# Kernel optimization log

Hardware: AMD Instinct MI355X
Metric: run time of the kernel (lower is better)

Reference implementation:

```python
import jax, jax.numpy as jnp
import numpy as np

B, L, C = 2, 2048, 1024
H = 16
D = C // H  # 64
MAX_SCALE_MUL = float(np.log(100.0))
EPS = 1e-12


def setup_inputs() -> dict:
    key = jax.random.key(0)
    ks = jax.random.split(key, 6)
    x = jax.random.normal(ks[0], (B, L, C), dtype=jnp.float32)
    attn_bias = jax.random.normal(ks[1], (1, 1, L, L), dtype=jnp.float32) * 0.02
    W_qkv = jax.random.normal(ks[2], (3 * C, C), dtype=jnp.float32) * (1.0 / np.sqrt(C))
    q_bias = jnp.zeros((C,), dtype=jnp.float32)
    v_bias = jnp.zeros((C,), dtype=jnp.float32)
    scale_mul = jnp.full((1, H, 1, 1), np.log(4.0), dtype=jnp.float32)
    W_proj = jax.random.normal(ks[3], (C, C), dtype=jnp.float32) * (1.0 / np.sqrt(C))
    b_proj = jnp.zeros((C,), dtype=jnp.float32)
    return {"x": x, "attn_bias": attn_bias, "W_qkv": W_qkv, "q_bias": q_bias,
            "v_bias": v_bias, "scale_mul": scale_mul, "W_proj": W_proj, "b_proj": b_proj}


def _l2norm(t):
    # F.normalize(dim=-1): x / max(||x||_2, eps)
    n = jnp.sqrt(jnp.sum(t * t, axis=-1, keepdims=True))
    return t / jnp.maximum(n, EPS)


def reference(x, attn_bias, W_qkv, q_bias, v_bias, scale_mul, W_proj, b_proj):
    bias = jnp.concatenate([q_bias, jnp.zeros_like(q_bias), v_bias])  # (3C,)
    qkv = x @ W_qkv.T + bias                     # (B, L, 3C)
    qkv = qkv.reshape(B, L, 3, H, D)
    q, k, v = jnp.moveaxis(qkv, 2, 0)            # each (B, L, H, D)
    q = jnp.transpose(q, (0, 2, 1, 3))           # (B, H, L, D)
    k = jnp.transpose(k, (0, 2, 1, 3))
    v = jnp.transpose(v, (0, 2, 1, 3))
    # attn_l2_norm path: scale = 1, learned per-head scale clamped at log(100)
    sm = jnp.exp(jnp.minimum(scale_mul, MAX_SCALE_MUL))  # (1, H, 1, 1)
    q = _l2norm(q) * sm
    k = _l2norm(k)
    scores = jnp.einsum('bhqd,bhkd->bhqk', q, k) + attn_bias  # scale=1
    attn = jax.nn.softmax(scores, axis=-1)
    out = jnp.einsum('bhqk,bhkd->bhqd', attn, v)  # (B, H, L, D)
    out = jnp.transpose(out, (0, 2, 1, 3)).reshape(B, L, C)
    return out @ W_proj.T + b_proj
```

## Files before the change

### kernel.cpp

```cpp
#include <hip/hip_runtime.h>


typedef __bf16 bf16x8 __attribute__((ext_vector_type(8)));
typedef __bf16 bf16x4 __attribute__((ext_vector_type(4)));
typedef float  f32x4  __attribute__((ext_vector_type(4)));

#define BB 2
#define LL 2048
#define CC 1024
#define HH 16
#define DD 64
#define LOG2E 1.44269504088896f

__device__ __forceinline__ f32x4 mfma_16x16x32(bf16x8 a, bf16x8 b, f32x4 c) {
    return __builtin_amdgcn_mfma_f32_16x16x32_bf16(a, b, c, 0, 0, 0);
}

__device__ __forceinline__ void gload_lds16(const __bf16* g, __bf16* lds) {
    __builtin_amdgcn_global_load_lds(
        (const __attribute__((address_space(1))) unsigned int*)g,
        (__attribute__((address_space(3))) unsigned int*)lds,
        16, 0, 0);
}

__device__ __forceinline__ unsigned pk_bf16(float a, float b) {
    unsigned short ua = __builtin_bit_cast(unsigned short, (__bf16)a);
    unsigned short ub = __builtin_bit_cast(unsigned short, (__bf16)b);
    return (unsigned)ua | ((unsigned)ub << 16);
}

__global__ __launch_bounds__(256) void cvt3_kernel(
    const float* __restrict__ x, const float* __restrict__ wq, const float* __restrict__ wp,
    __bf16* __restrict__ xb, __bf16* __restrict__ wqb, __bf16* __restrict__ wpb) {
    const int i = blockIdx.x * 256 + threadIdx.x;
    const float* src; __bf16* dst; int off;
    if (i < 1048576)      { src = x;  dst = xb;  off = i; }
    else if (i < 1835008) { src = wq; dst = wqb; off = i - 1048576; }
    else                  { src = wp; dst = wpb; off = i - 1835008; }
    float4 v = reinterpret_cast<const float4*>(src)[off];
    bf16x4 o;
    o[0] = (__bf16)v.x; o[1] = (__bf16)v.y; o[2] = (__bf16)v.z; o[3] = (__bf16)v.w;
    reinterpret_cast<bf16x4*>(dst)[off] = o;
}

__global__ __launch_bounds__(256) void gemm_qkv_fused_kernel(
    const __bf16* __restrict__ A, const __bf16* __restrict__ Bm,
    const float* __restrict__ q_bias, const float* __restrict__ v_bias,
    const float* __restrict__ scale_mul,
    __bf16* __restrict__ Qw, __bf16* __restrict__ Kw, __bf16* __restrict__ Vw) {
    __shared__ __bf16 As[128 * 64];
    __shared__ __bf16 Bs[128 * 64];
    const int tid = threadIdx.x;
    const int K = 1024;
    const int nwg = gridDim.x * gridDim.y;
    const int flat = blockIdx.y * gridDim.x + blockIdx.x;
    const int wg = (flat & 7) * (nwg >> 3) + (flat >> 3);
    const int m0 = (wg % gridDim.x) * 128, n0 = (wg / gridDim.x) * 128;
    const int w  = tid >> 6, l = tid & 63;
    const int wr = (w >> 1) * 64, wc = (w & 1) * 64;
    const int lr = l & 15, lg = l >> 4;
    const int rmask = (lr & 7) << 4;
    f32x4 acc[4][4] = {};
    const int lrow = l >> 3;
    const int celem = (((l & 7) ^ lrow) << 3);

    for (int kt = 0; kt < K; kt += 64) {
        __syncthreads();
#pragma unroll
        for (int i = 0; i < 4; ++i) {
            const int row = w * 32 + i * 8;
            gload_lds16(A + (size_t)(m0 + row + lrow) * K + kt + celem, &As[row * 64]);
            gload_lds16(Bm + (size_t)(n0 + row + lrow) * K + kt + celem, &Bs[row * 64]);
        }
        asm volatile("s_waitcnt vmcnt(0)" ::: "memory");
        __syncthreads();
#pragma unroll
        for (int kk = 0; kk < 2; ++kk) {
            bf16x8 af[4], bfr[4];
#pragma unroll
            for (int m = 0; m < 4; ++m)
                af[m] = *reinterpret_cast<const bf16x8*>(
                    (char*)As + (wr + m * 16 + lr) * 128 + ((kk * 64 + lg * 16) ^ rmask));
#pragma unroll
            for (int n = 0; n < 4; ++n)
                bfr[n] = *reinterpret_cast<const bf16x8*>(
                    (char*)Bs + (wc + n * 16 + lr) * 128 + ((kk * 64 + lg * 16) ^ rmask));
#pragma unroll
            for (int m = 0; m < 4; ++m)
#pragma unroll
                for (int n = 0; n < 4; ++n)
                    acc[m][n] = mfma_16x16x32(af[m], bfr[n], acc[m][n]);
        }
    }

    const int gcbase = n0 + wc;
    const int type = gcbase >> 10;
    const int h = (gcbase & 1023) >> 6;
    float qscale = 1.0f;
    if (type == 0) qscale = __expf(fminf(scale_mul[h], 4.60517019f)) * LOG2E;
    __bf16* dst = (type == 0) ? Qw : (type == 1) ? Kw : Vw;

#pragma unroll
    for (int m = 0; m < 4; ++m) {
        if (type != 1) {
            const float* bptr = (type == 0) ? q_bias : v_bias;
#pragma unroll
            for (int n = 0; n < 4; ++n) {
                float bv = bptr[(gcbase & 1023) + n * 16 + lr];
#pragma unroll
                for (int r = 0; r < 4; ++r) acc[m][n][r] += bv;
            }
        }
        float rs[4];
        if (type < 2) {
#pragma unroll
            for (int r = 0; r < 4; ++r) {
                float ss = 0.f;
#pragma unroll
                for (int n = 0; n < 4; ++n) ss += acc[m][n][r] * acc[m][n][r];
                rs[r] = ss;
            }
#pragma unroll
            for (int off = 1; off < 16; off <<= 1)
#pragma unroll
                for (int r = 0; r < 4; ++r) rs[r] += __shfl_xor(rs[r], off, 64);
#pragma unroll
            for (int r = 0; r < 4; ++r)
                rs[r] = ((type == 0) ? qscale : 1.0f) / fmaxf(sqrtf(rs[r]), 1e-12f);
        } else {
#pragma unroll
            for (int r = 0; r < 4; ++r) rs[r] = 1.0f;
        }
        const int rowg = m0 + wr + m * 16 + lg * 4;
#pragma unroll
        for (int n = 0; n < 4; ++n) {
            const int d = n * 16 + lr;
#pragma unroll
            for (int r = 0; r < 4; ++r) {
                const int row = rowg + r;
                const int bb = row >> 11, ll = row & 2047;
                dst[((size_t)((bb << 4) + h) * 2048 + ll) * 64 + d] =
                    (__bf16)(acc[m][n][r] * rs[r]);
            }
        }
    }
}

__global__ __launch_bounds__(256) void gemm_proj_kernel(
    const __bf16* __restrict__ A, const __bf16* __restrict__ Bm,
    float* __restrict__ Cf, const float* __restrict__ bias, int M, int N, int K) {
    __shared__ __bf16 As[128 * 64];
    __shared__ __bf16 Bs[128 * 64];
    const int tid = threadIdx.x;
    const int nwg = gridDim.x * gridDim.y;
    const int flat = blockIdx.y * gridDim.x + blockIdx.x;
    const int wg = (flat & 7) * (nwg >> 3) + (flat >> 3);
    const int m0 = (wg % gridDim.x) * 128, n0 = (wg / gridDim.x) * 128;
    const int w  = tid >> 6, l = tid & 63;
    const int wr = (w >> 1) * 64, wc = (w & 1) * 64;
    const int lr = l & 15, lg = l >> 4;
    const int rmask = (lr & 7) << 4;
    f32x4 acc[4][4] = {};
    const int lrow = l >> 3;
    const int celem = (((l & 7) ^ lrow) << 3);

    for (int kt = 0; kt < K; kt += 64) {
        __syncthreads();
#pragma unroll
        for (int i = 0; i < 4; ++i) {
            const int row = w * 32 + i * 8;
            gload_lds16(A + (size_t)(m0 + row + lrow) * K + kt + celem, &As[row * 64]);
            gload_lds16(Bm + (size_t)(n0 + row + lrow) * K + kt + celem, &Bs[row * 64]);
        }
        asm volatile("s_waitcnt vmcnt(0)" ::: "memory");
        __syncthreads();
#pragma unroll
        for (int kk = 0; kk < 2; ++kk) {
            bf16x8 af[4], bfr[4];
#pragma unroll
            for (int m = 0; m < 4; ++m)
                af[m] = *reinterpret_cast<const bf16x8*>(
                    (char*)As + (wr + m * 16 + lr) * 128 + ((kk * 64 + lg * 16) ^ rmask));
#pragma unroll
            for (int n = 0; n < 4; ++n)
                bfr[n] = *reinterpret_cast<const bf16x8*>(
                    (char*)Bs + (wc + n * 16 + lr) * 128 + ((kk * 64 + lg * 16) ^ rmask));
#pragma unroll
            for (int m = 0; m < 4; ++m)
#pragma unroll
                for (int n = 0; n < 4; ++n)
                    acc[m][n] = mfma_16x16x32(af[m], bfr[n], acc[m][n]);
        }
    }
#pragma unroll
    for (int m = 0; m < 4; ++m)
#pragma unroll
        for (int n = 0; n < 4; ++n) {
            const int row = m0 + wr + m * 16 + lg * 4;
            const int col = n0 + wc + n * 16 + lr;
#pragma unroll
            for (int r = 0; r < 4; ++r)
                Cf[(size_t)(row + r) * N + col] = acc[m][n][r] + bias[col];
        }
}

__global__ __launch_bounds__(256) void prep_kernel(
    const float* __restrict__ bias, __bf16* __restrict__ bias_bf,
    const __bf16* __restrict__ Vin, __bf16* __restrict__ Vp) {
    const int tid = threadIdx.x;
    if (blockIdx.x < 2048) {
        __shared__ float wmax[4];
        const int l = blockIdx.x;
        const int w = tid >> 6;
        float4 a = reinterpret_cast<const float4*>(bias + (size_t)l * 2048)[tid];
        float4 b = reinterpret_cast<const float4*>(bias + (size_t)l * 2048 + 1024)[tid];
        float m = fmaxf(fmaxf(fmaxf(a.x, a.y), fmaxf(a.z, a.w)),
                        fmaxf(fmaxf(b.x, b.y), fmaxf(b.z, b.w)));
#pragma unroll
        for (int off = 1; off < 64; off <<= 1) m = fmaxf(m, __shfl_xor(m, off, 64));
        if ((tid & 63) == 0) wmax[w] = m;
        __syncthreads();
        float M = fmaxf(fmaxf(wmax[0], wmax[1]), fmaxf(wmax[2], wmax[3]));
        bf16x4 o0, o1;
        o0[0] = (__bf16)((a.x - M) * LOG2E); o0[1] = (__bf16)((a.y - M) * LOG2E);
        o0[2] = (__bf16)((a.z - M) * LOG2E); o0[3] = (__bf16)((a.w - M) * LOG2E);
        o1[0] = (__bf16)((b.x - M) * LOG2E); o1[1] = (__bf16)((b.y - M) * LOG2E);
        o1[2] = (__bf16)((b.z - M) * LOG2E); o1[3] = (__bf16)((b.w - M) * LOG2E);
        reinterpret_cast<bf16x4*>(bias_bf + (size_t)l * 2048)[tid] = o0;
        reinterpret_cast<bf16x4*>(bias_bf + (size_t)l * 2048 + 1024)[tid] = o1;
    } else {
        __shared__ __bf16 T[64][72];
        const int idx = blockIdx.x - 2048;
        const int lb = idx & 31, bh = idx >> 5;
        const size_t base = (size_t)bh * LL * DD;
        const int row = tid >> 2, c = (tid & 3) * 16;
        {
            const __bf16* src = Vin + base + (size_t)(lb * 64 + row) * 64 + c;
            *reinterpret_cast<bf16x8*>(&T[row][c])     = *reinterpret_cast<const bf16x8*>(src);
            *reinterpret_cast<bf16x8*>(&T[row][c + 8]) = *reinterpret_cast<const bf16x8*>(src + 8);
        }
        __syncthreads();
        __bf16 val[16];
#pragma unroll
        for (int jj = 0; jj < 16; ++jj) {
            const int cp = c + jj;
            const int wb = cp & 31;
            const int kloc = (cp & ~31) | (((wb >> 3) & 3) << 2) | (((wb >> 2) & 1) << 4) | (wb & 3);
            val[jj] = T[kloc][row];
        }
        __bf16* dst = Vp + base + (size_t)row * 2048 + lb * 64 + c;
        *reinterpret_cast<bf16x8*>(dst)     = *reinterpret_cast<bf16x8*>(&val[0]);
        *reinterpret_cast<bf16x8*>(dst + 8) = *reinterpret_cast<bf16x8*>(&val[8]);
    }
}

__global__ __launch_bounds__(512, 6) void attn_kernel(
    const __bf16* __restrict__ Q, const __bf16* __restrict__ K,
    const __bf16* __restrict__ Vp, const __bf16* __restrict__ biasB,
    __bf16* __restrict__ Octx) {
    __shared__ __bf16 KVs[2][2][64 * 64];
    const int bh = blockIdx.x, qb = blockIdx.y;
    const int tid = threadIdx.x;
    const int w = tid >> 6, l = tid & 63;
    const int lr = l & 15, lg = l >> 4;
    const int rmask = (lr & 7) << 4;
    const int b = bh >> 4, h = bh & 15;
    const size_t base = (size_t)bh * LL * DD;

    const int gq = qb * 128 + w * 16 + lr;
    bf16x8 qf[2];
    qf[0] = *reinterpret_cast<const bf16x8*>(Q + base + (size_t)gq * 64 + lg * 8);
    qf[1] = *reinterpret_cast<const bf16x8*>(Q + base + (size_t)gq * 64 + 32 + lg * 8);
    const __bf16* brow = biasB + (size_t)gq * 2048 + lg * 4;

    bf16x8 ones;
#pragma unroll
    for (int j = 0; j < 8; ++j) ones[j] = (__bf16)1.0f;

    const int srow = w * 8 + (l >> 3);
    const int sce  = (l & 7) * 8;
    const int smask = (srow & 7) << 4;
    const __bf16* kgbase = K  + base + (size_t)srow * 64   + sce;
    const __bf16* vgbase = Vp + base + (size_t)srow * 2048 + sce;

    bf16x8 k0, v0;
    auto stage_regs = [&](int kb) {
        k0 = *reinterpret_cast<const bf16x8*>(kgbase + (size_t)kb * 64 * 64);
        v0 = *reinterpret_cast<const bf16x8*>(vgbase + kb * 64);
    };
    auto write_lds = [&](int buf) {
        *reinterpret_cast<bf16x8*>((char*)KVs[buf][0] + srow * 128 + ((sce * 2) ^ smask)) = k0;
        *reinterpret_cast<bf16x8*>((char*)KVs[buf][1] + srow * 128 + ((sce * 2) ^ smask)) = v0;
    };

    stage_regs(0);
    write_lds(0);

    f32x4 Oa[4] = {};
    f32x4 ls = {};
    int cur = 0;

    bf16x4 bcur[4];
#pragma unroll
    for (int t = 0; t < 4; ++t)
        bcur[t] = *reinterpret_cast<const bf16x4*>(brow + t * 16);

    for (int kb = 0; kb < 32; ++kb) {
        __syncthreads();
        if (kb < 31) stage_regs(kb + 1);

        bf16x4 bnext[4];
        if (kb < 31) {
#pragma unroll
            for (int t = 0; t < 4; ++t)
                bnext[t] = *reinterpret_cast<const bf16x4*>(brow + (kb + 1) * 64 + t * 16);
        }

        const char* Kc = (const char*)KVs[cur][0];
        const char* Vc = (const char*)KVs[cur][1];

        f32x4 sa[4];
#pragma unroll
        for (int t = 0; t < 4; ++t)
#pragma unroll
            for (int r = 0; r < 4; ++r)
                sa[t][r] = (float)bcur[t][r];

#pragma unroll
        for (int t = 0; t < 4; ++t) {
            const char* kr = Kc + (t * 16 + lr) * 128;
            bf16x8 kf0 = *reinterpret_cast<const bf16x8*>(kr + ((lg * 16) ^ rmask));
            bf16x8 kf1 = *reinterpret_cast<const bf16x8*>(kr + ((64 + lg * 16) ^ rmask));
            sa[t] = mfma_16x16x32(kf0, qf[0], sa[t]);
            sa[t] = mfma_16x16x32(kf1, qf[1], sa[t]);
        }

        float p[4][4];
#pragma unroll
        for (int t = 0; t < 4; ++t)
#pragma unroll
            for (int r = 0; r < 4; ++r)
                p[t][r] = exp2f(sa[t][r]);
        union Upa { unsigned u[4]; bf16x8 v; } pa0, pa1;
        pa0.u[0] = pk_bf16(p[0][0], p[0][1]); pa0.u[1] = pk_bf16(p[0][2], p[0][3]);
        pa0.u[2] = pk_bf16(p[1][0], p[1][1]); pa0.u[3] = pk_bf16(p[1][2], p[1][3]);
        pa1.u[0] = pk_bf16(p[2][0], p[2][1]); pa1.u[1] = pk_bf16(p[2][2], p[2][3]);
        pa1.u[2] = pk_bf16(p[3][0], p[3][1]); pa1.u[3] = pk_bf16(p[3][2], p[3][3]);

        ls = mfma_16x16x32(pa0.v, ones, ls);
        ls = mfma_16x16x32(pa1.v, ones, ls);

#pragma unroll
        for (int t = 0; t < 4; ++t) {
            const char* vr = Vc + (t * 16 + lr) * 128;
            bf16x8 vf0 = *reinterpret_cast<const bf16x8*>(vr + ((lg * 16) ^ rmask));
            bf16x8 vf1 = *reinterpret_cast<const bf16x8*>(vr + ((64 + lg * 16) ^ rmask));
            Oa[t] = mfma_16x16x32(pa0.v, vf0, Oa[t]);
            Oa[t] = mfma_16x16x32(pa1.v, vf1, Oa[t]);
        }

        if (kb < 31) {
            write_lds(cur ^ 1);
#pragma unroll
            for (int t = 0; t < 4; ++t) bcur[t] = bnext[t];
        }
        cur ^= 1;
    }

    float inv[4];
#pragma unroll
    for (int r = 0; r < 4; ++r) inv[r] = 1.0f / ls[r];
#pragma unroll
    for (int t = 0; t < 4; ++t)
#pragma unroll
        for (int r = 0; r < 4; ++r) {
            const int row = qb * 128 + w * 16 + lg * 4 + r;
            Octx[((size_t)(b * 2048 + row)) * 1024 + h * 64 + t * 16 + lr] =
                (__bf16)(Oa[t][r] * inv[r]);
        }
}

extern "C" void kernel_launch(void* const* d_in, const int* in_sizes, int n_in,
                              void* d_out, int out_size, void* d_ws, size_t ws_size,
                              hipStream_t stream) {
    const float* x         = (const float*)d_in[0];
    const float* attn_bias = (const float*)d_in[1];
    const float* W_qkv     = (const float*)d_in[2];
    const float* q_bias    = (const float*)d_in[3];
    const float* v_bias    = (const float*)d_in[4];
    const float* scale_mul = (const float*)d_in[5];
    const float* W_proj    = (const float*)d_in[6];
    const float* b_proj    = (const float*)d_in[7];
    float* out = (float*)d_out;

    char* ws = (char*)d_ws;
    size_t off = 0;
    auto alloc = [&](size_t bytes) {
        void* p = ws + off;
        off = (off + bytes + 255) & ~(size_t)255;
        return p;
    };
    __bf16* Vw      = (__bf16*)alloc((size_t)BB * HH * LL * DD * 2);
    __bf16* xb      = (__bf16*)alloc((size_t)4096 * 1024 * 2);
    __bf16* wqkvb   = (__bf16*)alloc((size_t)3072 * 1024 * 2);
    __bf16* wprojb  = (__bf16*)alloc((size_t)1024 * 1024 * 2);
    __bf16* Qw      = (__bf16*)alloc((size_t)BB * HH * LL * DD * 2);
    __bf16* Kw      = (__bf16*)alloc((size_t)BB * HH * LL * DD * 2);
    __bf16* Oc      = (__bf16*)alloc((size_t)4096 * 1024 * 2);
    __bf16* biasB   = (__bf16*)alloc((size_t)2048 * 2048 * 2);
    __bf16* Vp      = (__bf16*)alloc((size_t)BB * HH * LL * DD * 2);

    cvt3_kernel<<<8192, 256, 0, stream>>>(x, W_qkv, W_proj, xb, wqkvb, wprojb);

    gemm_qkv_fused_kernel<<<dim3(32, 24), 256, 0, stream>>>(
        xb, wqkvb, q_bias, v_bias, scale_mul, Qw, Kw, Vw);

    prep_kernel<<<3072, 256, 0, stream>>>(attn_bias, biasB, Vw, Vp);

    attn_kernel<<<dim3(32, 16), 512, 0, stream>>>(Qw, Kw, Vp, biasB, Oc);

    gemm_proj_kernel<<<dim3(32, 8), 256, 0, stream>>>(
        Oc, wprojb, out, b_proj, 4096, 1024, 1024);
}
```

Baseline: 167.5 us.

## Write V in permuted transposed layout from QKV GEMM epilogue and drop prep kernel

The QKV GEMM epilogue now writes V straight into the transposed, key-permuted layout the attention kernel consumes, so the separate V transpose pass and its intermediate buffer go away. The attention-bias conversion moves into the input conversion kernel as extra blocks, which removes one launch. Together these cut a kernel launch and a full read/write of V. The trade-off is that V stores from the epilogue become scattered 8-byte writes with a large stride, which may coalesce poorly.

```diff
diff --git a/kernel.cpp b/kernel.cpp
--- a/kernel.cpp
+++ b/kernel.cpp
@@ -29,25 +29,50 @@
     return (unsigned)ua | ((unsigned)ub << 16);
 }
 
-__global__ __launch_bounds__(256) void cvt3_kernel(
+__global__ __launch_bounds__(256) void cvt3b_kernel(
     const float* __restrict__ x, const float* __restrict__ wq, const float* __restrict__ wp,
-    __bf16* __restrict__ xb, __bf16* __restrict__ wqb, __bf16* __restrict__ wpb) {
-    const int i = blockIdx.x * 256 + threadIdx.x;
-    const float* src; __bf16* dst; int off;
-    if (i < 1048576)      { src = x;  dst = xb;  off = i; }
-    else if (i < 1835008) { src = wq; dst = wqb; off = i - 1048576; }
-    else                  { src = wp; dst = wpb; off = i - 1835008; }
-    float4 v = reinterpret_cast<const float4*>(src)[off];
-    bf16x4 o;
-    o[0] = (__bf16)v.x; o[1] = (__bf16)v.y; o[2] = (__bf16)v.z; o[3] = (__bf16)v.w;
-    reinterpret_cast<bf16x4*>(dst)[off] = o;
+    const float* __restrict__ bias,
+    __bf16* __restrict__ xb, __bf16* __restrict__ wqb, __bf16* __restrict__ wpb,
+    __bf16* __restrict__ bias_bf) {
+    const int tid = threadIdx.x;
+    if (blockIdx.x < 8192) {
+        const int i = blockIdx.x * 256 + tid;
+        const float* src; __bf16* dst; int off;
+        if (i < 1048576)      { src = x;  dst = xb;  off = i; }
+        else if (i < 1835008) { src = wq; dst = wqb; off = i - 1048576; }
+        else                  { src = wp; dst = wpb; off = i - 1835008; }
+        float4 v = reinterpret_cast<const float4*>(src)[off];
+        bf16x4 o;
+        o[0] = (__bf16)v.x; o[1] = (__bf16)v.y; o[2] = (__bf16)v.z; o[3] = (__bf16)v.w;
+        reinterpret_cast<bf16x4*>(dst)[off] = o;
+    } else {
+        __shared__ float wmax[4];
+        const int l = blockIdx.x - 8192;
+        const int w = tid >> 6;
+        float4 a = reinterpret_cast<const float4*>(bias + (size_t)l * 2048)[tid];
+        float4 b = reinterpret_cast<const float4*>(bias + (size_t)l * 2048 + 1024)[tid];
+        float m = fmaxf(fmaxf(fmaxf(a.x, a.y), fmaxf(a.z, a.w)),
+                        fmaxf(fmaxf(b.x, b.y), fmaxf(b.z, b.w)));
+#pragma unroll
+        for (int off = 1; off < 64; off <<= 1) m = fmaxf(m, __shfl_xor(m, off, 64));
+        if ((tid & 63) == 0) wmax[w] = m;
+        __syncthreads();
+        float M = fmaxf(fmaxf(wmax[0], wmax[1]), fmaxf(wmax[2], wmax[3]));
+        bf16x4 o0, o1;
+        o0[0] = (__bf16)((a.x - M) * LOG2E); o0[1] = (__bf16)((a.y - M) * LOG2E);
+        o0[2] = (__bf16)((a.z - M) * LOG2E); o0[3] = (__bf16)((a.w - M) * LOG2E);
+        o1[0] = (__bf16)((b.x - M) * LOG2E); o1[1] = (__bf16)((b.y - M) * LOG2E);
+        o1[2] = (__bf16)((b.z - M) * LOG2E); o1[3] = (__bf16)((b.w - M) * LOG2E);
+        reinterpret_cast<bf16x4*>(bias_bf + (size_t)l * 2048)[tid] = o0;
+        reinterpret_cast<bf16x4*>(bias_bf + (size_t)l * 2048 + 1024)[tid] = o1;
+    }
 }
 
 __global__ __launch_bounds__(256) void gemm_qkv_fused_kernel(
     const __bf16* __restrict__ A, const __bf16* __restrict__ Bm,
     const float* __restrict__ q_bias, const float* __restrict__ v_bias,
     const float* __restrict__ scale_mul,
-    __bf16* __restrict__ Qw, __bf16* __restrict__ Kw, __bf16* __restrict__ Vw) {
+    __bf16* __restrict__ Qw, __bf16* __restrict__ Kw, __bf16* __restrict__ Vp) {
     __shared__ __bf16 As[128 * 64];
     __shared__ __bf16 Bs[128 * 64];
     const int tid = threadIdx.x;
@@ -98,7 +123,7 @@
     const int h = (gcbase & 1023) >> 6;
     float qscale = 1.0f;
     if (type == 0) qscale = __expf(fminf(scale_mul[h], 4.60517019f)) * LOG2E;
-    __bf16* dst = (type == 0) ? Qw : (type == 1) ? Kw : Vw;
+    __bf16* dst = (type == 0) ? Qw : Kw;
 
 #pragma unroll
     for (int m = 0; m < 4; ++m) {
@@ -111,8 +136,9 @@
                 for (int r = 0; r < 4; ++r) acc[m][n][r] += bv;
             }
         }
-        float rs[4];
+        const int rowg = m0 + wr + m * 16 + lg * 4;
         if (type < 2) {
+            float rs[4];
 #pragma unroll
             for (int r = 0; r < 4; ++r) {
                 float ss = 0.f;
@@ -127,20 +153,28 @@
 #pragma unroll
             for (int r = 0; r < 4; ++r)
                 rs[r] = ((type == 0) ? qscale : 1.0f) / fmaxf(sqrtf(rs[r]), 1e-12f);
+#pragma unroll
+            for (int n = 0; n < 4; ++n) {
+                const int d = n * 16 + lr;
+#pragma unroll
+                for (int r = 0; r < 4; ++r) {
+                    const int row = rowg + r;
+                    const int bb = row >> 11, ll = row & 2047;
+                    dst[((size_t)((bb << 4) + h) * 2048 + ll) * 64 + d] =
+                        (__bf16)(acc[m][n][r] * rs[r]);
+                }
+            }
         } else {
-#pragma unroll
-            for (int r = 0; r < 4; ++r) rs[r] = 1.0f;
-        }
-        const int rowg = m0 + wr + m * 16 + lg * 4;
-#pragma unroll
-        for (int n = 0; n < 4; ++n) {
-            const int d = n * 16 + lr;
-#pragma unroll
-            for (int r = 0; r < 4; ++r) {
-                const int row = rowg + r;
-                const int bb = row >> 11, ll = row & 2047;
-                dst[((size_t)((bb << 4) + h) * 2048 + ll) * 64 + d] =
-                    (__bf16)(acc[m][n][r] * rs[r]);
+            const int bb = rowg >> 11, ll0 = rowg & 2047;
+            const int posb = (ll0 & ~31) | (((ll0 >> 2) & 3) << 3) | (((ll0 >> 4) & 1) << 2);
+#pragma unroll
+            for (int n = 0; n < 4; ++n) {
+                const int d = n * 16 + lr;
+                bf16x4 vv;
+#pragma unroll
+                for (int r = 0; r < 4; ++r) vv[r] = (__bf16)acc[m][n][r];
+                *reinterpret_cast<bf16x4*>(
+                    Vp + ((size_t)((bb << 4) + h) * 64 + d) * 2048 + posb) = vv;
             }
         }
     }
@@ -204,56 +238,6 @@
         }
 }
 
-__global__ __launch_bounds__(256) void prep_kernel(
-    const float* __restrict__ bias, __bf16* __restrict__ bias_bf,
-    const __bf16* __restrict__ Vin, __bf16* __restrict__ Vp) {
-    const int tid = threadIdx.x;
-    if (blockIdx.x < 2048) {
-        __shared__ float wmax[4];
-        const int l = blockIdx.x;
-        const int w = tid >> 6;
-        float4 a = reinterpret_cast<const float4*>(bias + (size_t)l * 2048)[tid];
-        float4 b = reinterpret_cast<const float4*>(bias + (size_t)l * 2048 + 1024)[tid];
-        float m = fmaxf(fmaxf(fmaxf(a.x, a.y), fmaxf(a.z, a.w)),
-                        fmaxf(fmaxf(b.x, b.y), fmaxf(b.z, b.w)));
-#pragma unroll
-        for (int off = 1; off < 64; off <<= 1) m = fmaxf(m, __shfl_xor(m, off, 64));
-        if ((tid & 63) == 0) wmax[w] = m;
-        __syncthreads();
-        float M = fmaxf(fmaxf(wmax[0], wmax[1]), fmaxf(wmax[2], wmax[3]));
-        bf16x4 o0, o1;
-        o0[0] = (__bf16)((a.x - M) * LOG2E); o0[1] = (__bf16)((a.y - M) * LOG2E);
-        o0[2] = (__bf16)((a.z - M) * LOG2E); o0[3] = (__bf16)((a.w - M) * LOG2E);
-        o1[0] = (__bf16)((b.x - M) * LOG2E); o1[1] = (__bf16)((b.y - M) * LOG2E);
-        o1[2] = (__bf16)((b.z - M) * LOG2E); o1[3] = (__bf16)((b.w - M) * LOG2E);
-        reinterpret_cast<bf16x4*>(bias_bf + (size_t)l * 2048)[tid] = o0;
-        reinterpret_cast<bf16x4*>(bias_bf + (size_t)l * 2048 + 1024)[tid] = o1;
-    } else {
-        __shared__ __bf16 T[64][72];
-        const int idx = blockIdx.x - 2048;
-        const int lb = idx & 31, bh = idx >> 5;
-        const size_t base = (size_t)bh * LL * DD;
-        const int row = tid >> 2, c = (tid & 3) * 16;
-        {
-            const __bf16* src = Vin + base + (size_t)(lb * 64 + row) * 64 + c;
-            *reinterpret_cast<bf16x8*>(&T[row][c])     = *reinterpret_cast<const bf16x8*>(src);
-            *reinterpret_cast<bf16x8*>(&T[row][c + 8]) = *reinterpret_cast<const bf16x8*>(src + 8);
-        }
-        __syncthreads();
-        __bf16 val[16];
-#pragma unroll
-        for (int jj = 0; jj < 16; ++jj) {
-            const int cp = c + jj;
-            const int wb = cp & 31;
-            const int kloc = (cp & ~31) | (((wb >> 3) & 3) << 2) | (((wb >> 2) & 1) << 4) | (wb & 3);
-            val[jj] = T[kloc][row];
-        }
-        __bf16* dst = Vp + base + (size_t)row * 2048 + lb * 64 + c;
-        *reinterpret_cast<bf16x8*>(dst)     = *reinterpret_cast<bf16x8*>(&val[0]);
-        *reinterpret_cast<bf16x8*>(dst + 8) = *reinterpret_cast<bf16x8*>(&val[8]);
-    }
-}
-
 __global__ __launch_bounds__(512, 6) void attn_kernel(
     const __bf16* __restrict__ Q, const __bf16* __restrict__ K,
     const __bf16* __restrict__ Vp, const __bf16* __restrict__ biasB,
@@ -400,7 +384,6 @@
         off = (off + bytes + 255) & ~(size_t)255;
         return p;
     };
-    __bf16* Vw      = (__bf16*)alloc((size_t)BB * HH * LL * DD * 2);
     __bf16* xb      = (__bf16*)alloc((size_t)4096 * 1024 * 2);
     __bf16* wqkvb   = (__bf16*)alloc((size_t)3072 * 1024 * 2);
     __bf16* wprojb  = (__bf16*)alloc((size_t)1024 * 1024 * 2);
@@ -410,12 +393,11 @@
     __bf16* biasB   = (__bf16*)alloc((size_t)2048 * 2048 * 2);
     __bf16* Vp      = (__bf16*)alloc((size_t)BB * HH * LL * DD * 2);
 
-    cvt3_kernel<<<8192, 256, 0, stream>>>(x, W_qkv, W_proj, xb, wqkvb, wprojb);
+    cvt3b_kernel<<<10240, 256, 0, stream>>>(x, W_qkv, W_proj, attn_bias,
+                                            xb, wqkvb, wprojb, biasB);
 
     gemm_qkv_fused_kernel<<<dim3(32, 24), 256, 0, stream>>>(
-        xb, wqkvb, q_bias, v_bias, scale_mul, Qw, Kw, Vw);
-
-    prep_kernel<<<3072, 256, 0, stream>>>(attn_bias, biasB, Vw, Vp);
+        xb, wqkvb, q_bias, v_bias, scale_mul, Qw, Kw, Vp);
 
     attn_kernel<<<dim3(32, 16), 512, 0, stream>>>(Qw, Kw, Vp, biasB, Oc);
 
```

Measured after the change: 163.0 us (median of 2 runs). 2.7% less time.
